# Kernel tuning notes

Measured on AMD Instinct MI355X. Metric: run time of the kernel, lower is better.

The kernel has to match this reference:

```python
import jax, jax.numpy as jnp
import numpy as np

NEG_SLOPE = 0.01  # torch F.leaky_relu default
NUM_USER, NUM_ITEM, DIM = 50000, 30000, 64
N_NODES = NUM_USER + NUM_ITEM
N_INTER = 800000
N_LAYERS = 2


def _leaky(x):
    return jax.nn.leaky_relu(x, NEG_SLOPE)


def _gcn_tower(features, preference, id_embedding, W, b, row, col):
    # x = cat(preference, features); F.normalize (L2 per row)
    x = jnp.concatenate([preference, features], axis=0)  # [N, 64]
    x = x / jnp.maximum(jnp.linalg.norm(x, axis=1, keepdims=True), 1e-12)
    deg = jax.ops.segment_sum(jnp.ones(row.shape, x.dtype), row, num_segments=N_NODES)  # bincount(row)
    for i in range(N_LAYERS):
        # Abstract_GCN: scatter-mean of gathered neighbor feats, then linear
        agg = jax.ops.segment_sum(x[col], row, num_segments=N_NODES) / deg[:, None]
        h = _leaky(agg @ W[i, 0].T + b[i, 0])
        # has_id=True, concate=False
        x_hat = _leaky(x @ W[i, 1].T + b[i, 1]) + id_embedding
        x = _leaky(h @ W[i, 2].T + b[i, 2] + x_hat)
    return x


def setup_inputs() -> dict:
    key = jax.random.key(0)
    ks = jax.random.split(key, 14)
    # bipartite user->item edges with full node coverage (every node appears
    # as a row after symmetrization, matching real interaction data where
    # bincount(row) has no zeros)
    r1 = jnp.arange(NUM_USER, dtype=jnp.int64 if jax.config.jax_enable_x64 else jnp.int32)
    c1 = jax.random.randint(ks[0], (NUM_USER,), NUM_USER, N_NODES)
    r2 = jax.random.randint(ks[1], (NUM_ITEM,), 0, NUM_USER)
    c2 = NUM_USER + jnp.arange(NUM_ITEM, dtype=r1.dtype)
    rest = N_INTER - NUM_USER - NUM_ITEM
    r3 = jax.random.randint(ks[2], (rest,), 0, NUM_USER)
    c3 = jax.random.randint(ks[3], (rest,), NUM_USER, N_NODES)
    row0 = jnp.concatenate([r1, r2, r3])
    col0 = jnp.concatenate([c1, c2, c3])
    # symmetrize: cat(edge_index, edge_index[[1,0]])
    edge_index = jnp.stack([jnp.concatenate([row0, col0]),
                            jnp.concatenate([col0, row0])])  # [2, 1.6M]
    s = 0.1  # xavier-ish scale for 64x64
    return {
        "v_feat": jax.random.normal(ks[4], (NUM_ITEM, DIM), jnp.float32),
        "t_feat": jax.random.normal(ks[5], (NUM_ITEM, DIM), jnp.float32),
        "id_embedding": jax.random.normal(ks[6], (N_NODES, DIM), jnp.float32) * s,
        "v_pref": jax.random.normal(ks[7], (NUM_USER, DIM), jnp.float32) * s,
        "t_pref": jax.random.normal(ks[8], (NUM_USER, DIM), jnp.float32) * s,
        "v_W": jax.random.normal(ks[9], (N_LAYERS, 3, DIM, DIM), jnp.float32) * s,
        "v_b": jnp.zeros((N_LAYERS, 3, DIM), jnp.float32),
        "t_W": jax.random.normal(ks[10], (N_LAYERS, 3, DIM, DIM), jnp.float32) * s,
        "t_b": jnp.zeros((N_LAYERS, 3, DIM), jnp.float32),
        "edge_index": edge_index,
    }


def reference(v_feat, t_feat, id_embedding, v_pref, t_pref, v_W, v_b, t_W, t_b, edge_index):
    row, col = edge_index[0], edge_index[1]
    rep_v = _gcn_tower(v_feat, v_pref, id_embedding, v_W, v_b, row, col)
    rep_t = _gcn_tower(t_feat, t_pref, id_embedding, t_W, t_b, row, col)
    return (rep_v + rep_t) / 2.0  # MMGCN.get_rep representation
```

## Files before the change

kernel.cpp:

```cpp
#include <hip/hip_runtime.h>
#include <hip/hip_bf16.h>

#define NUM_USER 50000
#define N_NODES  80000
#define DIM      64
#define NEG_SLOPE 0.01f

#define NB 313
#define BSHIFT 8
#define RMASK 255
#define CSHIFT 17
#define CMASK 0x1FFFF
#define CAP 10240

typedef __attribute__((ext_vector_type(8))) short short8;
typedef __attribute__((ext_vector_type(4))) float f32x4;

typedef unsigned short XT;

__device__ __forceinline__ float leaky(float v) {
    return v > 0.0f ? v : v * NEG_SLOPE;
}

__device__ __forceinline__ int load_idx(const void* ei, int is64, long long pos) {
    if (is64) return (int)((const long long*)ei)[pos];
    return ((const int*)ei)[pos];
}
__device__ __forceinline__ float load_f(const void* p, int isbf16, size_t i) {
    if (isbf16) return __bfloat162float(((const __hip_bfloat16*)p)[i]);
    return ((const float*)p)[i];
}

__device__ __forceinline__ unsigned short f2bf(float f) {
    unsigned u = __float_as_uint(f);
    u += 0x7fffu + ((u >> 16) & 1u);
    return (unsigned short)(u >> 16);
}

__device__ __forceinline__ void acc8(float* a, uint4 r) {
    a[0] += __uint_as_float(r.x << 16);
    a[1] += __uint_as_float(r.x & 0xffff0000u);
    a[2] += __uint_as_float(r.y << 16);
    a[3] += __uint_as_float(r.y & 0xffff0000u);
    a[4] += __uint_as_float(r.z << 16);
    a[5] += __uint_as_float(r.z & 0xffff0000u);
    a[6] += __uint_as_float(r.w << 16);
    a[7] += __uint_as_float(r.w & 0xffff0000u);
}

__global__ void detect_kernel(const unsigned int* __restrict__ feat_words,
                              const int* __restrict__ ei_words,
                              int* __restrict__ flags,
                              int* __restrict__ bucketCur) {
    int lane = threadIdx.x & 63;
    for (int i = lane; i < 320; i += 64) bucketCur[i] = 0;
    int orv = 0;
    for (int i = lane * 2 + 1; i < 1024; i += 128) orv |= ei_words[i];
    int hits = 0;
    for (int i = lane; i < 256; i += 64) {
        unsigned e = (feat_words[i] >> 7) & 0xFF;
        hits += (e == 126 || e == 127) ? 1 : 0;
    }
    #pragma unroll
    for (int d = 32; d > 0; d >>= 1) {
        orv  |= __shfl_xor(orv, d, 64);
        hits += __shfl_xor(hits, d, 64);
    }
    if (lane == 0 && blockIdx.x == 0) {
        flags[0] = (orv == 0) ? 1 : 0;
        flags[1] = (hits > 64) ? 1 : 0;
    }
}

__global__ __launch_bounds__(256) void megafuse_kernel(
        const void* __restrict__ ei, int E, int binBlocks, int initBlocks,
        const int* __restrict__ flags,
        int* __restrict__ bucketCur, unsigned int* __restrict__ recs,
        const void* __restrict__ vp, const void* __restrict__ tp,
        const void* __restrict__ vf, const void* __restrict__ tf,
        XT* __restrict__ xc,
        const void* __restrict__ vW, const void* __restrict__ tW,
        const void* __restrict__ vb, const void* __restrict__ tb,
        unsigned short* __restrict__ Wbf, float* __restrict__ bfp) {
    if ((int)blockIdx.x < binBlocks) {
        __shared__ int bloc[320];
        __shared__ int bres[320];
        int tid = threadIdx.x;
        for (int i = tid; i < 320; i += 256) bloc[i] = 0;
        __syncthreads();
        int is64 = flags[0];
        long long base = (long long)blockIdx.x * 2048;
        int bb[8], cc[8], lp[8], rl[8];
        #pragma unroll
        for (int it = 0; it < 8; ++it) {
            bb[it] = -1;
            long long e = base + it * 256 + tid;
            if (e < E) {
                int r = load_idx(ei, is64, e);
                int c = load_idx(ei, is64, (long long)E + e);
                if ((unsigned)r < N_NODES && (unsigned)c < N_NODES) {
                    int b = r >> BSHIFT;
                    bb[it] = b;
                    cc[it] = c;
                    rl[it] = r & RMASK;
                    lp[it] = atomicAdd(&bloc[b], 1);
                }
            }
        }
        __syncthreads();
        for (int i = tid; i < NB; i += 256) {
            int v = bloc[i];
            bres[i] = v ? atomicAdd(&bucketCur[i], v) : 0;
        }
        __syncthreads();
        #pragma unroll
        for (int it = 0; it < 8; ++it) {
            if (bb[it] >= 0) {
                int pos = bres[bb[it]] + lp[it];
                if (pos < CAP)
                    recs[(size_t)bb[it] * CAP + pos] =
                        ((unsigned)rl[it] << CSHIFT) | (unsigned)cc[it];
            }
        }
    } else if ((int)blockIdx.x < binBlocks + initBlocks) {
        int n = (blockIdx.x - binBlocks) * 4 + (threadIdx.x >> 6);
        if (n >= N_NODES) return;
        int lane = threadIdx.x & 63;
        int isb = flags[1];
        float a, b;
        if (n < NUM_USER) {
            a = load_f(vp, isb, (size_t)n * DIM + lane);
            b = load_f(tp, isb, (size_t)n * DIM + lane);
        } else {
            a = load_f(vf, isb, (size_t)(n - NUM_USER) * DIM + lane);
            b = load_f(tf, isb, (size_t)(n - NUM_USER) * DIM + lane);
        }
        float sa = a * a, sb = b * b;
        #pragma unroll
        for (int d = 32; d > 0; d >>= 1) {
            sa += __shfl_xor(sa, d, 64);
            sb += __shfl_xor(sb, d, 64);
        }
        float ra = 1.0f / fmaxf(sqrtf(sa), 1e-12f);
        float rb = 1.0f / fmaxf(sqrtf(sb), 1e-12f);
        xc[(size_t)n * 128 + lane]      = f2bf(a * ra);
        xc[(size_t)n * 128 + 64 + lane] = f2bf(b * rb);
    } else {
        int isb = flags[1];
        int j = (blockIdx.x - binBlocks - initBlocks) * 256 + threadIdx.x;
        if (j < 2 * 24576) {
            int tw = j / 24576, r = j % 24576;
            Wbf[j] = f2bf(load_f(tw ? tW : vW, isb, r));
        } else if (j < 2 * 24576 + 2 * 384) {
            int i2 = j - 2 * 24576;
            int tw = i2 / 384, r = i2 % 384;
            bfp[i2] = load_f(tw ? tb : vb, isb, r);
        }
    }
}

__global__ __launch_bounds__(512) void bin2csr_kernel(
        const unsigned int* __restrict__ recs,
        const int* __restrict__ bucketCur,
        int* __restrict__ cnt, int* __restrict__ cur,
        int* __restrict__ csr) {
    __shared__ int rcnt[256];
    __shared__ int sc[256];
    __shared__ int lcur[256];
    int b = blockIdx.x;
    int t = threadIdx.x;
    int base = b * CAP;
    int count = bucketCur[b];
    if (count > CAP) count = CAP;

    if (t < 256) { rcnt[t] = 0; lcur[t] = 0; }
    __syncthreads();
    for (int i = t; i < count; i += 512) {
        unsigned rec = recs[(size_t)base + i];
        atomicAdd(&rcnt[rec >> CSHIFT], 1);
    }
    __syncthreads();
    int v = (t < 256) ? rcnt[t] : 0;
    if (t < 256) sc[t] = v;
    __syncthreads();
    for (int d = 1; d < 256; d <<= 1) {
        int x = 0;
        if (t < 256) { x = sc[t]; if (t >= d) x += sc[t - d]; }
        __syncthreads();
        if (t < 256) sc[t] = x;
        __syncthreads();
    }
    if (t < 256) {
        int row = (b << BSHIFT) + t;
        if (row < N_NODES) {
            cnt[row] = v;
            cur[row] = base + sc[t];
        }
    }
    __syncthreads();
    for (int i = t; i < count; i += 512) {
        unsigned rec = recs[(size_t)base + i];
        int rloc = rec >> CSHIFT;
        int c = rec & CMASK;
        int pos = base + (sc[rloc] - rcnt[rloc]) + atomicAdd(&lcur[rloc], 1);
        csr[pos] = c;
    }
}

__global__ __launch_bounds__(512) void gather_kernel(
        const XT* __restrict__ xc, XT* __restrict__ agg,
        const int* __restrict__ cnt, const int* __restrict__ cur,
        const int* __restrict__ csr) {
    int n = blockIdx.x * 8 + (threadIdx.x >> 6);
    if (n >= N_NODES) return;
    int lane = threadIdx.x & 63;
    int g8 = lane >> 3;
    int s  = lane & 7;
    int gg = g8 >> 1;
    int h  = g8 & 1;

    int d = cnt[n];
    int base = cur[n] - d;
    const int* nb = csr + base;
    const XT* xh = xc + h * 64;

    float acc[8];
    #pragma unroll
    for (int f = 0; f < 8; ++f) acc[f] = 0.f;

    int jj = gg;
    for (; jj + 4 < d; jj += 8) {
        int c0 = nb[jj];
        int c1 = nb[jj + 4];
        uint4 r0 = ((const uint4*)(xh + (size_t)c0 * 128))[s];
        uint4 r1 = ((const uint4*)(xh + (size_t)c1 * 128))[s];
        acc8(acc, r0);
        acc8(acc, r1);
    }
    if (jj < d) {
        int c0 = nb[jj];
        uint4 r0 = ((const uint4*)(xh + (size_t)c0 * 128))[s];
        acc8(acc, r0);
    }

    #pragma unroll
    for (int dd = 16; dd < 64; dd <<= 1) {
        #pragma unroll
        for (int f = 0; f < 8; ++f) acc[f] += __shfl_xor(acc[f], dd, 64);
    }

    float invd = (d > 0) ? 1.0f / (float)d : 0.0f;
    if (g8 < 2) {
        uint4 w;
        w.x = (unsigned)f2bf(acc[0] * invd) | ((unsigned)f2bf(acc[1] * invd) << 16);
        w.y = (unsigned)f2bf(acc[2] * invd) | ((unsigned)f2bf(acc[3] * invd) << 16);
        w.z = (unsigned)f2bf(acc[4] * invd) | ((unsigned)f2bf(acc[5] * invd) << 16);
        w.w = (unsigned)f2bf(acc[6] * invd) | ((unsigned)f2bf(acc[7] * invd) << 16);
        ((uint4*)(agg + (size_t)n * 128 + h * 64))[s] = w;
    }
}

__global__ __launch_bounds__(256) void dense_mfma_kernel(
        XT* __restrict__ xc, const XT* __restrict__ agg,
        void* __restrict__ out, int last,
        const void* __restrict__ id_emb,
        const unsigned short* __restrict__ Wbf, const float* __restrict__ bfp,
        int layer, const int* __restrict__ flags) {
    __shared__ unsigned short hts[4][16 * 72];
    int wave = threadIdx.x >> 6, lane = threadIdx.x & 63;
    int quad = lane >> 4, l16 = lane & 15;
    int isb = flags[1];
    int n0 = (blockIdx.x * 4 + wave) * 16;
    unsigned short* ht = hts[wave];

    float xres[2][16];
    float idv[16];

    #pragma unroll
    for (int tw = 0; tw < 2; ++tw) {
        int toff = tw * 64;
        const unsigned short* Wm = Wbf + (size_t)((tw * 2 + layer) * 3) * 4096;
        const float* bb = bfp + (tw * 2 + layer) * 192;
        size_t arow = (size_t)(n0 + l16) * 128 + toff + quad * 8;

        short8 a0, a1;
        f32x4 accP[4];

        a0 = *(const short8*)(xc + arow);
        a1 = *(const short8*)(xc + arow + 32);
        #pragma unroll
        for (int t = 0; t < 4; ++t) {
            f32x4 c = {0.f, 0.f, 0.f, 0.f};
            short8 b0 = *(const short8*)(Wm + 4096 + (16 * t + l16) * 64 + quad * 8);
            short8 b1 = *(const short8*)(Wm + 4096 + (16 * t + l16) * 64 + 32 + quad * 8);
            c = __builtin_amdgcn_mfma_f32_16x16x32_bf16(a0, b0, c, 0, 0, 0);
            c = __builtin_amdgcn_mfma_f32_16x16x32_bf16(a1, b1, c, 0, 0, 0);
            float bias = bb[64 + 16 * t + l16];
            #pragma unroll
            for (int r = 0; r < 4; ++r) accP[t][r] = leaky(c[r] + bias);
        }

        a0 = *(const short8*)(agg + arow);
        a1 = *(const short8*)(agg + arow + 32);
        #pragma unroll
        for (int t = 0; t < 4; ++t) {
            f32x4 c = {0.f, 0.f, 0.f, 0.f};
            short8 b0 = *(const short8*)(Wm + (16 * t + l16) * 64 + quad * 8);
            short8 b1 = *(const short8*)(Wm + (16 * t + l16) * 64 + 32 + quad * 8);
            c = __builtin_amdgcn_mfma_f32_16x16x32_bf16(a0, b0, c, 0, 0, 0);
            c = __builtin_amdgcn_mfma_f32_16x16x32_bf16(a1, b1, c, 0, 0, 0);
            float bias = bb[16 * t + l16];
            #pragma unroll
            for (int r = 0; r < 4; ++r)
                ht[(quad * 4 + r) * 72 + 16 * t + l16] = f2bf(leaky(c[r] + bias));
        }

        a0 = *(const short8*)(ht + l16 * 72 + quad * 8);
        a1 = *(const short8*)(ht + l16 * 72 + 32 + quad * 8);
        #pragma unroll
        for (int t = 0; t < 4; ++t) {
            f32x4 c = {0.f, 0.f, 0.f, 0.f};
            short8 b0 = *(const short8*)(Wm + 2 * 4096 + (16 * t + l16) * 64 + quad * 8);
            short8 b1 = *(const short8*)(Wm + 2 * 4096 + (16 * t + l16) * 64 + 32 + quad * 8);
            c = __builtin_amdgcn_mfma_f32_16x16x32_bf16(a0, b0, c, 0, 0, 0);
            c = __builtin_amdgcn_mfma_f32_16x16x32_bf16(a1, b1, c, 0, 0, 0);
            float bias = bb[128 + 16 * t + l16];
            #pragma unroll
            for (int r = 0; r < 4; ++r) {
                int node2 = n0 + quad * 4 + r;
                int j = 16 * t + l16;
                if (tw == 0)
                    idv[t * 4 + r] = load_f(id_emb, isb, (size_t)node2 * 64 + j);
                xres[tw][t * 4 + r] = leaky(c[r] + bias + accP[t][r] + idv[t * 4 + r]);
            }
        }
    }

    if (!last) {
        #pragma unroll
        for (int tw = 0; tw < 2; ++tw) {
            #pragma unroll
            for (int t = 0; t < 4; ++t) {
                #pragma unroll
                for (int r = 0; r < 4; ++r) {
                    int node2 = n0 + quad * 4 + r;
                    int j = 16 * t + l16;
                    xc[(size_t)node2 * 128 + tw * 64 + j] = f2bf(xres[tw][t * 4 + r]);
                }
            }
        }
    } else {
        #pragma unroll
        for (int t = 0; t < 4; ++t) {
            #pragma unroll
            for (int r = 0; r < 4; ++r) {
                int node2 = n0 + quad * 4 + r;
                int j = 16 * t + l16;
                float avg = (xres[0][t * 4 + r] + xres[1][t * 4 + r]) * 0.5f;
                if (isb) ((unsigned short*)out)[(size_t)node2 * 64 + j] = f2bf(avg);
                else     ((float*)out)[(size_t)node2 * 64 + j] = avg;
            }
        }
    }
}

extern "C" void kernel_launch(void* const* d_in, const int* in_sizes, int n_in,
                              void* d_out, int out_size, void* d_ws, size_t ws_size,
                              hipStream_t stream) {
    const void* v_feat = d_in[0];
    const void* t_feat = d_in[1];
    const void* id_emb = d_in[2];
    const void* v_pref = d_in[3];
    const void* t_pref = d_in[4];
    const void* v_W    = d_in[5];
    const void* v_b    = d_in[6];
    const void* t_W    = d_in[7];
    const void* t_b    = d_in[8];
    const void* ei     = d_in[9];

    const int E = in_sizes[9] / 2;
    char* ws = (char*)d_ws;

    size_t o = 0;
    int*            flags     = (int*)(ws + o);            o += 16;
    int*            cnt       = (int*)(ws + o);            o += 320000;
    int*            cur       = (int*)(ws + o);            o += 320000;
    int*            bucketCur = (int*)(ws + o);            o += 320 * 4;
    unsigned short* Wbf       = (unsigned short*)(ws + o); o += 2 * 24576 * 2;
    float*          bfp       = (float*)(ws + o);          o += 2 * 384 * 4;
    XT* xc  = (XT*)(ws + o); o += (size_t)N_NODES * 128 * sizeof(XT);
    XT* agg = (XT*)(ws + o); o += (size_t)N_NODES * 128 * sizeof(XT);
    unsigned int* recs = (unsigned int*)(ws + o); o += (size_t)NB * CAP * 4;
    int* csr = (int*)(ws + o);

    detect_kernel<<<dim3(1), dim3(64), 0, stream>>>(
        (const unsigned int*)v_feat, (const int*)ei, flags, bucketCur);

    const int binBlocks  = (E + 2047) / 2048;
    const int initBlocks = (N_NODES + 3) / 4;
    const int packBlocks = (2 * 24576 + 2 * 384 + 255) / 256;
    megafuse_kernel<<<dim3(binBlocks + initBlocks + packBlocks), dim3(256), 0, stream>>>(
        ei, E, binBlocks, initBlocks, flags, bucketCur, recs,
        v_pref, t_pref, v_feat, t_feat, xc,
        v_W, t_W, v_b, t_b, Wbf, bfp);

    bin2csr_kernel<<<dim3(NB), dim3(512), 0, stream>>>(recs, bucketCur, cnt, cur, csr);

    const int gatherBlocks = (N_NODES + 7) / 8;
    const int denseBlocks  = N_NODES / (16 * 4);

    gather_kernel<<<dim3(gatherBlocks), dim3(512), 0, stream>>>(xc, agg, cnt, cur, csr);
    dense_mfma_kernel<<<dim3(denseBlocks), dim3(256), 0, stream>>>(
        xc, agg, d_out, 0, id_emb, Wbf, bfp, 0, flags);
    gather_kernel<<<dim3(gatherBlocks), dim3(512), 0, stream>>>(xc, agg, cnt, cur, csr);
    dense_mfma_kernel<<<dim3(denseBlocks), dim3(256), 0, stream>>>(
        xc, agg, d_out, 1, id_emb, Wbf, bfp, 1, flags);
}
```

Before: 365.4 us.

## Fuse neighbor gather into dense MFMA layer kernel with ping-pong buffers

Merges the gather (scatter-mean) kernel into the dense MFMA kernel. Each wave aggregates its 16 nodes into shared memory, then runs the linear layers directly from LDS. Features are double-buffered (xcA/xcB) because other blocks may still be reading the old features while the layer writes new ones. This removes the agg round trip through global memory and two launches. The cost is less gather parallelism per node, since each wave now handles 16 nodes in sequence. Also widens bin2csr to 1024 threads, and adds a redundant bias store line.

After: 458.4 us. +25.5%, slower.

```diff
diff --git a/kernel.cpp b/kernel.cpp
--- a/kernel.cpp
+++ b/kernel.cpp
@@ -154,12 +154,12 @@
         } else if (j < 2 * 24576 + 2 * 384) {
             int i2 = j - 2 * 24576;
             int tw = i2 / 384, r = i2 % 384;
-            bfp[i2] = load_f(tw ? tb : vb, isb, r);
-        }
-    }
-}
-
-__global__ __launch_bounds__(512) void bin2csr_kernel(
+            bfp[i2] = f2bf(0.0f), bfp[i2] = load_f(tw ? tb : vb, isb, r);
+        }
+    }
+}
+
+__global__ __launch_bounds__(1024) void bin2csr_kernel(
         const unsigned int* __restrict__ recs,
         const int* __restrict__ bucketCur,
         int* __restrict__ cnt, int* __restrict__ cur,
@@ -175,7 +175,7 @@
 
     if (t < 256) { rcnt[t] = 0; lcur[t] = 0; }
     __syncthreads();
-    for (int i = t; i < count; i += 512) {
+    for (int i = t; i < count; i += 1024) {
         unsigned rec = recs[(size_t)base + i];
         atomicAdd(&rcnt[rec >> CSHIFT], 1);
     }
@@ -198,7 +198,7 @@
         }
     }
     __syncthreads();
-    for (int i = t; i < count; i += 512) {
+    for (int i = t; i < count; i += 1024) {
         unsigned rec = recs[(size_t)base + i];
         int rloc = rec >> CSHIFT;
         int c = rec & CMASK;
@@ -207,74 +207,73 @@
     }
 }
 
-__global__ __launch_bounds__(512) void gather_kernel(
-        const XT* __restrict__ xc, XT* __restrict__ agg,
-        const int* __restrict__ cnt, const int* __restrict__ cur,
-        const int* __restrict__ csr) {
-    int n = blockIdx.x * 8 + (threadIdx.x >> 6);
-    if (n >= N_NODES) return;
-    int lane = threadIdx.x & 63;
-    int g8 = lane >> 3;
-    int s  = lane & 7;
-    int gg = g8 >> 1;
-    int h  = g8 & 1;
-
-    int d = cnt[n];
-    int base = cur[n] - d;
-    const int* nb = csr + base;
-    const XT* xh = xc + h * 64;
-
-    float acc[8];
-    #pragma unroll
-    for (int f = 0; f < 8; ++f) acc[f] = 0.f;
-
-    int jj = gg;
-    for (; jj + 4 < d; jj += 8) {
-        int c0 = nb[jj];
-        int c1 = nb[jj + 4];
-        uint4 r0 = ((const uint4*)(xh + (size_t)c0 * 128))[s];
-        uint4 r1 = ((const uint4*)(xh + (size_t)c1 * 128))[s];
-        acc8(acc, r0);
-        acc8(acc, r1);
-    }
-    if (jj < d) {
-        int c0 = nb[jj];
-        uint4 r0 = ((const uint4*)(xh + (size_t)c0 * 128))[s];
-        acc8(acc, r0);
-    }
-
-    #pragma unroll
-    for (int dd = 16; dd < 64; dd <<= 1) {
-        #pragma unroll
-        for (int f = 0; f < 8; ++f) acc[f] += __shfl_xor(acc[f], dd, 64);
-    }
-
-    float invd = (d > 0) ? 1.0f / (float)d : 0.0f;
-    if (g8 < 2) {
-        uint4 w;
-        w.x = (unsigned)f2bf(acc[0] * invd) | ((unsigned)f2bf(acc[1] * invd) << 16);
-        w.y = (unsigned)f2bf(acc[2] * invd) | ((unsigned)f2bf(acc[3] * invd) << 16);
-        w.z = (unsigned)f2bf(acc[4] * invd) | ((unsigned)f2bf(acc[5] * invd) << 16);
-        w.w = (unsigned)f2bf(acc[6] * invd) | ((unsigned)f2bf(acc[7] * invd) << 16);
-        ((uint4*)(agg + (size_t)n * 128 + h * 64))[s] = w;
-    }
-}
-
-__global__ __launch_bounds__(256) void dense_mfma_kernel(
-        XT* __restrict__ xc, const XT* __restrict__ agg,
+__global__ __launch_bounds__(256) void layer_fused_kernel(
+        const XT* __restrict__ xin, XT* __restrict__ xout,
         void* __restrict__ out, int last,
         const void* __restrict__ id_emb,
         const unsigned short* __restrict__ Wbf, const float* __restrict__ bfp,
+        const int* __restrict__ cnt, const int* __restrict__ cur,
+        const int* __restrict__ csr,
         int layer, const int* __restrict__ flags) {
+    __shared__ unsigned short aggs[4][16 * 136];
     __shared__ unsigned short hts[4][16 * 72];
     int wave = threadIdx.x >> 6, lane = threadIdx.x & 63;
     int quad = lane >> 4, l16 = lane & 15;
     int isb = flags[1];
     int n0 = (blockIdx.x * 4 + wave) * 16;
-    unsigned short* ht = hts[wave];
-
-    float xres[2][16];
-    float idv[16];
+    unsigned short* agg = aggs[wave];
+    unsigned short* ht  = hts[wave];
+
+    {
+        int g8 = lane >> 3;
+        int s  = lane & 7;
+        int gg = g8 >> 1;
+        int h  = g8 & 1;
+        const XT* xh = xin + h * 64;
+
+        for (int k = 0; k < 16; ++k) {
+            int node = n0 + k;
+            int d = cnt[node];
+            int base = cur[node] - d;
+            const int* nb = csr + base;
+
+            float acc[8];
+            #pragma unroll
+            for (int f = 0; f < 8; ++f) acc[f] = 0.f;
+
+            int jj = gg;
+            for (; jj + 4 < d; jj += 8) {
+                int c0 = nb[jj];
+                int c1 = nb[jj + 4];
+                uint4 r0 = ((const uint4*)(xh + (size_t)c0 * 128))[s];
+                uint4 r1 = ((const uint4*)(xh + (size_t)c1 * 128))[s];
+                acc8(acc, r0);
+                acc8(acc, r1);
+            }
+            if (jj < d) {
+                uint4 r0 = ((const uint4*)(xh + (size_t)nb[jj] * 128))[s];
+                acc8(acc, r0);
+            }
+
+            #pragma unroll
+            for (int dd = 16; dd < 64; dd <<= 1) {
+                #pragma unroll
+                for (int f = 0; f < 8; ++f) acc[f] += __shfl_xor(acc[f], dd, 64);
+            }
+
+            float invd = (d > 0) ? 1.0f / (float)d : 0.0f;
+            if (g8 < 2) {
+                uint4 w;
+                w.x = (unsigned)f2bf(acc[0] * invd) | ((unsigned)f2bf(acc[1] * invd) << 16);
+                w.y = (unsigned)f2bf(acc[2] * invd) | ((unsigned)f2bf(acc[3] * invd) << 16);
+                w.z = (unsigned)f2bf(acc[4] * invd) | ((unsigned)f2bf(acc[5] * invd) << 16);
+                w.w = (unsigned)f2bf(acc[6] * invd) | ((unsigned)f2bf(acc[7] * invd) << 16);
+                *(uint4*)(agg + k * 136 + h * 64 + s * 8) = w;
+            }
+        }
+    }
+
+    float res0[16];
 
     #pragma unroll
     for (int tw = 0; tw < 2; ++tw) {
@@ -286,8 +285,8 @@
         short8 a0, a1;
         f32x4 accP[4];
 
-        a0 = *(const short8*)(xc + arow);
-        a1 = *(const short8*)(xc + arow + 32);
+        a0 = *(const short8*)(xin + arow);
+        a1 = *(const short8*)(xin + arow + 32);
         #pragma unroll
         for (int t = 0; t < 4; ++t) {
             f32x4 c = {0.f, 0.f, 0.f, 0.f};
@@ -300,8 +299,8 @@
             for (int r = 0; r < 4; ++r) accP[t][r] = leaky(c[r] + bias);
         }
 
-        a0 = *(const short8*)(agg + arow);
-        a1 = *(const short8*)(agg + arow + 32);
+        a0 = *(const short8*)(agg + l16 * 136 + toff + quad * 8);
+        a1 = *(const short8*)(agg + l16 * 136 + toff + 32 + quad * 8);
         #pragma unroll
         for (int t = 0; t < 4; ++t) {
             f32x4 c = {0.f, 0.f, 0.f, 0.f};
@@ -329,36 +328,17 @@
             for (int r = 0; r < 4; ++r) {
                 int node2 = n0 + quad * 4 + r;
                 int j = 16 * t + l16;
-                if (tw == 0)
-                    idv[t * 4 + r] = load_f(id_emb, isb, (size_t)node2 * 64 + j);
-                xres[tw][t * 4 + r] = leaky(c[r] + bias + accP[t][r] + idv[t * 4 + r]);
-            }
-        }
-    }
-
-    if (!last) {
-        #pragma unroll
-        for (int tw = 0; tw < 2; ++tw) {
-            #pragma unroll
-            for (int t = 0; t < 4; ++t) {
-                #pragma unroll
-                for (int r = 0; r < 4; ++r) {
-                    int node2 = n0 + quad * 4 + r;
-                    int j = 16 * t + l16;
-                    xc[(size_t)node2 * 128 + tw * 64 + j] = f2bf(xres[tw][t * 4 + r]);
+                float idv = load_f(id_emb, isb, (size_t)node2 * 64 + j);
+                float v = leaky(c[r] + bias + accP[t][r] + idv);
+                if (!last) {
+                    xout[(size_t)node2 * 128 + toff + j] = f2bf(v);
+                } else if (tw == 0) {
+                    res0[t * 4 + r] = v;
+                } else {
+                    float avg = (res0[t * 4 + r] + v) * 0.5f;
+                    if (isb) ((unsigned short*)out)[(size_t)node2 * 64 + j] = f2bf(avg);
+                    else     ((float*)out)[(size_t)node2 * 64 + j] = avg;
                 }
-            }
-        }
-    } else {
-        #pragma unroll
-        for (int t = 0; t < 4; ++t) {
-            #pragma unroll
-            for (int r = 0; r < 4; ++r) {
-                int node2 = n0 + quad * 4 + r;
-                int j = 16 * t + l16;
-                float avg = (xres[0][t * 4 + r] + xres[1][t * 4 + r]) * 0.5f;
-                if (isb) ((unsigned short*)out)[(size_t)node2 * 64 + j] = f2bf(avg);
-                else     ((float*)out)[(size_t)node2 * 64 + j] = avg;
             }
         }
     }
@@ -388,8 +368,8 @@
     int*            bucketCur = (int*)(ws + o);            o += 320 * 4;
     unsigned short* Wbf       = (unsigned short*)(ws + o); o += 2 * 24576 * 2;
     float*          bfp       = (float*)(ws + o);          o += 2 * 384 * 4;
-    XT* xc  = (XT*)(ws + o); o += (size_t)N_NODES * 128 * sizeof(XT);
-    XT* agg = (XT*)(ws + o); o += (size_t)N_NODES * 128 * sizeof(XT);
+    XT* xcA = (XT*)(ws + o); o += (size_t)N_NODES * 128 * sizeof(XT);
+    XT* xcB = (XT*)(ws + o); o += (size_t)N_NODES * 128 * sizeof(XT);
     unsigned int* recs = (unsigned int*)(ws + o); o += (size_t)NB * CAP * 4;
     int* csr = (int*)(ws + o);
 
@@ -401,18 +381,15 @@
     const int packBlocks = (2 * 24576 + 2 * 384 + 255) / 256;
     megafuse_kernel<<<dim3(binBlocks + initBlocks + packBlocks), dim3(256), 0, stream>>>(
         ei, E, binBlocks, initBlocks, flags, bucketCur, recs,
-        v_pref, t_pref, v_feat, t_feat, xc,
+        v_pref, t_pref, v_feat, t_feat, xcA,
         v_W, t_W, v_b, t_b, Wbf, bfp);
 
-    bin2csr_kernel<<<dim3(NB), dim3(512), 0, stream>>>(recs, bucketCur, cnt, cur, csr);
-
-    const int gatherBlocks = (N_NODES + 7) / 8;
-    const int denseBlocks  = N_NODES / (16 * 4);
-
-    gather_kernel<<<dim3(gatherBlocks), dim3(512), 0, stream>>>(xc, agg, cnt, cur, csr);
-    dense_mfma_kernel<<<dim3(denseBlocks), dim3(256), 0, stream>>>(
-        xc, agg, d_out, 0, id_emb, Wbf, bfp, 0, flags);
-    gather_kernel<<<dim3(gatherBlocks), dim3(512), 0, stream>>>(xc, agg, cnt, cur, csr);
-    dense_mfma_kernel<<<dim3(denseBlocks), dim3(256), 0, stream>>>(
-        xc, agg, d_out, 1, id_emb, Wbf, bfp, 1, flags);
-}
+    bin2csr_kernel<<<dim3(NB), dim3(1024), 0, stream>>>(recs, bucketCur, cnt, cur, csr);
+
+    const int layerBlocks = N_NODES / (16 * 4);
+
+    layer_fused_kernel<<<dim3(layerBlocks), dim3(256), 0, stream>>>(
+        xcA, xcB, d_out, 0, id_emb, Wbf, bfp, cnt, cur, csr, 0, flags);
+    layer_fused_kernel<<<dim3(layerBlocks), dim3(256), 0, stream>>>(
+        xcB, xcA, d_out, 1, id_emb, Wbf, bfp, cnt, cur, csr, 1, flags);
+}
```

## Regroup prep kernels and pre-convert id embedding to bf16

Applied to the files above, without the earlier changes.

Splits the edge binning into its own kernel and merges the bucket-to-CSR pass with feature normalization and weight packing in one 512-thread launch. The independent init and pack work can then overlap with CSR construction. When workspace allows, the id embedding is also converted to bf16 once so the dense kernels read half the bytes. This adds an 80000x64 conversion pass and rounds id_embedding to bf16, which slightly lowers precision.

After: 381.3 us. 1.04x slower.

```diff
diff --git a/kernel.cpp b/kernel.cpp
--- a/kernel.cpp
+++ b/kernel.cpp
@@ -35,6 +35,9 @@
     unsigned u = __float_as_uint(f);
     u += 0x7fffu + ((u >> 16) & 1u);
     return (unsigned short)(u >> 16);
+}
+__device__ __forceinline__ float bf2f(unsigned short v) {
+    return __uint_as_float(((unsigned)v) << 16);
 }
 
 __device__ __forceinline__ void acc8(float* a, uint4 r) {
@@ -72,58 +75,108 @@
     }
 }
 
-__global__ __launch_bounds__(256) void megafuse_kernel(
-        const void* __restrict__ ei, int E, int binBlocks, int initBlocks,
+__global__ __launch_bounds__(256) void binplace_kernel(
+        const void* __restrict__ ei, int E,
         const int* __restrict__ flags,
-        int* __restrict__ bucketCur, unsigned int* __restrict__ recs,
+        int* __restrict__ bucketCur, unsigned int* __restrict__ recs) {
+    __shared__ int bloc[320];
+    __shared__ int bres[320];
+    int tid = threadIdx.x;
+    for (int i = tid; i < 320; i += 256) bloc[i] = 0;
+    __syncthreads();
+    int is64 = flags[0];
+    long long base = (long long)blockIdx.x * 2048;
+    int bb[8], cc[8], lp[8], rl[8];
+    #pragma unroll
+    for (int it = 0; it < 8; ++it) {
+        bb[it] = -1;
+        long long e = base + it * 256 + tid;
+        if (e < E) {
+            int r = load_idx(ei, is64, e);
+            int c = load_idx(ei, is64, (long long)E + e);
+            if ((unsigned)r < N_NODES && (unsigned)c < N_NODES) {
+                int b = r >> BSHIFT;
+                bb[it] = b;
+                cc[it] = c;
+                rl[it] = r & RMASK;
+                lp[it] = atomicAdd(&bloc[b], 1);
+            }
+        }
+    }
+    __syncthreads();
+    for (int i = tid; i < NB; i += 256) {
+        int v = bloc[i];
+        bres[i] = v ? atomicAdd(&bucketCur[i], v) : 0;
+    }
+    __syncthreads();
+    #pragma unroll
+    for (int it = 0; it < 8; ++it) {
+        if (bb[it] >= 0) {
+            int pos = bres[bb[it]] + lp[it];
+            if (pos < CAP)
+                recs[(size_t)bb[it] * CAP + pos] =
+                    ((unsigned)rl[it] << CSHIFT) | (unsigned)cc[it];
+        }
+    }
+}
+
+__global__ __launch_bounds__(512) void prep2_kernel(
+        const unsigned int* __restrict__ recs, const int* __restrict__ bucketCur,
+        int* __restrict__ cnt, int* __restrict__ cur, int* __restrict__ csr,
+        int initBlocks, const int* __restrict__ flags,
         const void* __restrict__ vp, const void* __restrict__ tp,
         const void* __restrict__ vf, const void* __restrict__ tf,
         XT* __restrict__ xc,
         const void* __restrict__ vW, const void* __restrict__ tW,
         const void* __restrict__ vb, const void* __restrict__ tb,
-        unsigned short* __restrict__ Wbf, float* __restrict__ bfp) {
-    if ((int)blockIdx.x < binBlocks) {
-        __shared__ int bloc[320];
-        __shared__ int bres[320];
-        int tid = threadIdx.x;
-        for (int i = tid; i < 320; i += 256) bloc[i] = 0;
+        unsigned short* __restrict__ Wbf, float* __restrict__ bfp,
+        const void* __restrict__ id_emb, unsigned short* __restrict__ idbf,
+        int useIdbf) {
+    int bx = blockIdx.x;
+    if (bx < NB) {
+        __shared__ int rcnt[256];
+        __shared__ int sc[256];
+        __shared__ int lcur[256];
+        int b = bx;
+        int t = threadIdx.x;
+        int base = b * CAP;
+        int count = bucketCur[b];
+        if (count > CAP) count = CAP;
+
+        if (t < 256) { rcnt[t] = 0; lcur[t] = 0; }
         __syncthreads();
-        int is64 = flags[0];
-        long long base = (long long)blockIdx.x * 2048;
-        int bb[8], cc[8], lp[8], rl[8];
-        #pragma unroll
-        for (int it = 0; it < 8; ++it) {
-            bb[it] = -1;
-            long long e = base + it * 256 + tid;
-            if (e < E) {
-                int r = load_idx(ei, is64, e);
-                int c = load_idx(ei, is64, (long long)E + e);
-                if ((unsigned)r < N_NODES && (unsigned)c < N_NODES) {
-                    int b = r >> BSHIFT;
-                    bb[it] = b;
-                    cc[it] = c;
-                    rl[it] = r & RMASK;
-                    lp[it] = atomicAdd(&bloc[b], 1);
-                }
+        for (int i = t; i < count; i += 512) {
+            unsigned rec = recs[(size_t)base + i];
+            atomicAdd(&rcnt[rec >> CSHIFT], 1);
+        }
+        __syncthreads();
+        int v = (t < 256) ? rcnt[t] : 0;
+        if (t < 256) sc[t] = v;
+        __syncthreads();
+        for (int d = 1; d < 256; d <<= 1) {
+            int x = 0;
+            if (t < 256) { x = sc[t]; if (t >= d) x += sc[t - d]; }
+            __syncthreads();
+            if (t < 256) sc[t] = x;
+            __syncthreads();
+        }
+        if (t < 256) {
+            int row = (b << BSHIFT) + t;
+            if (row < N_NODES) {
+                cnt[row] = v;
+                cur[row] = base + sc[t];
             }
         }
         __syncthreads();
-        for (int i = tid; i < NB; i += 256) {
-            int v = bloc[i];
-            bres[i] = v ? atomicAdd(&bucketCur[i], v) : 0;
-        }
-        __syncthreads();
-        #pragma unroll
-        for (int it = 0; it < 8; ++it) {
-            if (bb[it] >= 0) {
-                int pos = bres[bb[it]] + lp[it];
-                if (pos < CAP)
-                    recs[(size_t)bb[it] * CAP + pos] =
-                        ((unsigned)rl[it] << CSHIFT) | (unsigned)cc[it];
-            }
-        }
-    } else if ((int)blockIdx.x < binBlocks + initBlocks) {
-        int n = (blockIdx.x - binBlocks) * 4 + (threadIdx.x >> 6);
+        for (int i = t; i < count; i += 512) {
+            unsigned rec = recs[(size_t)base + i];
+            int rloc = rec >> CSHIFT;
+            int c = rec & CMASK;
+            int pos = base + (sc[rloc] - rcnt[rloc]) + atomicAdd(&lcur[rloc], 1);
+            csr[pos] = c;
+        }
+    } else if (bx < NB + initBlocks) {
+        int n = (bx - NB) * 8 + (threadIdx.x >> 6);
         if (n >= N_NODES) return;
         int lane = threadIdx.x & 63;
         int isb = flags[1];
@@ -147,7 +200,7 @@
         xc[(size_t)n * 128 + 64 + lane] = f2bf(b * rb);
     } else {
         int isb = flags[1];
-        int j = (blockIdx.x - binBlocks - initBlocks) * 256 + threadIdx.x;
+        int j = (bx - NB - initBlocks) * 512 + threadIdx.x;
         if (j < 2 * 24576) {
             int tw = j / 24576, r = j % 24576;
             Wbf[j] = f2bf(load_f(tw ? tW : vW, isb, r));
@@ -155,55 +208,11 @@
             int i2 = j - 2 * 24576;
             int tw = i2 / 384, r = i2 % 384;
             bfp[i2] = load_f(tw ? tb : vb, isb, r);
-        }
-    }
-}
-
-__global__ __launch_bounds__(512) void bin2csr_kernel(
-        const unsigned int* __restrict__ recs,
-        const int* __restrict__ bucketCur,
-        int* __restrict__ cnt, int* __restrict__ cur,
-        int* __restrict__ csr) {
-    __shared__ int rcnt[256];
-    __shared__ int sc[256];
-    __shared__ int lcur[256];
-    int b = blockIdx.x;
-    int t = threadIdx.x;
-    int base = b * CAP;
-    int count = bucketCur[b];
-    if (count > CAP) count = CAP;
-
-    if (t < 256) { rcnt[t] = 0; lcur[t] = 0; }
-    __syncthreads();
-    for (int i = t; i < count; i += 512) {
-        unsigned rec = recs[(size_t)base + i];
-        atomicAdd(&rcnt[rec >> CSHIFT], 1);
-    }
-    __syncthreads();
-    int v = (t < 256) ? rcnt[t] : 0;
-    if (t < 256) sc[t] = v;
-    __syncthreads();
-    for (int d = 1; d < 256; d <<= 1) {
-        int x = 0;
-        if (t < 256) { x = sc[t]; if (t >= d) x += sc[t - d]; }
-        __syncthreads();
-        if (t < 256) sc[t] = x;
-        __syncthreads();
-    }
-    if (t < 256) {
-        int row = (b << BSHIFT) + t;
-        if (row < N_NODES) {
-            cnt[row] = v;
-            cur[row] = base + sc[t];
-        }
-    }
-    __syncthreads();
-    for (int i = t; i < count; i += 512) {
-        unsigned rec = recs[(size_t)base + i];
-        int rloc = rec >> CSHIFT;
-        int c = rec & CMASK;
-        int pos = base + (sc[rloc] - rcnt[rloc]) + atomicAdd(&lcur[rloc], 1);
-        csr[pos] = c;
+        } else if (useIdbf) {
+            int k = j - (2 * 24576 + 2 * 384);
+            if (k < N_NODES * DIM)
+                idbf[k] = f2bf(load_f(id_emb, isb, (size_t)k));
+        }
     }
 }
 
@@ -263,7 +272,7 @@
 __global__ __launch_bounds__(256) void dense_mfma_kernel(
         XT* __restrict__ xc, const XT* __restrict__ agg,
         void* __restrict__ out, int last,
-        const void* __restrict__ id_emb,
+        const void* __restrict__ id_emb, const unsigned short* __restrict__ idbf,
         const unsigned short* __restrict__ Wbf, const float* __restrict__ bfp,
         int layer, const int* __restrict__ flags) {
     __shared__ unsigned short hts[4][16 * 72];
@@ -330,7 +339,8 @@
                 int node2 = n0 + quad * 4 + r;
                 int j = 16 * t + l16;
                 if (tw == 0)
-                    idv[t * 4 + r] = load_f(id_emb, isb, (size_t)node2 * 64 + j);
+                    idv[t * 4 + r] = idbf ? bf2f(idbf[(size_t)node2 * 64 + j])
+                                          : load_f(id_emb, isb, (size_t)node2 * 64 + j);
                 xres[tw][t * 4 + r] = leaky(c[r] + bias + accP[t][r] + idv[t * 4 + r]);
             }
         }
@@ -391,28 +401,38 @@
     XT* xc  = (XT*)(ws + o); o += (size_t)N_NODES * 128 * sizeof(XT);
     XT* agg = (XT*)(ws + o); o += (size_t)N_NODES * 128 * sizeof(XT);
     unsigned int* recs = (unsigned int*)(ws + o); o += (size_t)NB * CAP * 4;
-    int* csr = (int*)(ws + o);
+    int* csr = (int*)(ws + o);                     o += (size_t)NB * CAP * 4;
+    unsigned short* idbf = nullptr;
+    int useIdbf = 0;
+    if (o + (size_t)N_NODES * DIM * 2 <= ws_size) {
+        idbf = (unsigned short*)(ws + o);
+        useIdbf = 1;
+    }
 
     detect_kernel<<<dim3(1), dim3(64), 0, stream>>>(
         (const unsigned int*)v_feat, (const int*)ei, flags, bucketCur);
 
-    const int binBlocks  = (E + 2047) / 2048;
-    const int initBlocks = (N_NODES + 3) / 4;
-    const int packBlocks = (2 * 24576 + 2 * 384 + 255) / 256;
-    megafuse_kernel<<<dim3(binBlocks + initBlocks + packBlocks), dim3(256), 0, stream>>>(
-        ei, E, binBlocks, initBlocks, flags, bucketCur, recs,
+    const int binBlocks = (E + 2047) / 2048;
+    binplace_kernel<<<dim3(binBlocks), dim3(256), 0, stream>>>(
+        ei, E, flags, bucketCur, recs);
+
+    const int initBlocks = (N_NODES + 7) / 8;
+    const int packElems  = 2 * 24576 + 2 * 384 + (useIdbf ? N_NODES * DIM : 0);
+    const int packBlocks = (packElems + 511) / 512;
+    prep2_kernel<<<dim3(NB + initBlocks + packBlocks), dim3(512), 0, stream>>>(
+        recs, bucketCur, cnt, cur, csr,
+        initBlocks, flags,
         v_pref, t_pref, v_feat, t_feat, xc,
-        v_W, t_W, v_b, t_b, Wbf, bfp);
-
-    bin2csr_kernel<<<dim3(NB), dim3(512), 0, stream>>>(recs, bucketCur, cnt, cur, csr);
+        v_W, t_W, v_b, t_b, Wbf, bfp,
+        id_emb, idbf, useIdbf);
 
     const int gatherBlocks = (N_NODES + 7) / 8;
     const int denseBlocks  = N_NODES / (16 * 4);
 
     gather_kernel<<<dim3(gatherBlocks), dim3(512), 0, stream>>>(xc, agg, cnt, cur, csr);
     dense_mfma_kernel<<<dim3(denseBlocks), dim3(256), 0, stream>>>(
-        xc, agg, d_out, 0, id_emb, Wbf, bfp, 0, flags);
+        xc, agg, d_out, 0, id_emb, idbf, Wbf, bfp, 0, flags);
     gather_kernel<<<dim3(gatherBlocks), dim3(512), 0, stream>>>(xc, agg, cnt, cur, csr);
     dense_mfma_kernel<<<dim3(denseBlocks), dim3(256), 0, stream>>>(
-        xc, agg, d_out, 1, id_emb, Wbf, bfp, 1, flags);
-}
+        xc, agg, d_out, 1, id_emb, idbf, Wbf, bfp, 1, flags);
+}
```

## Split dense MFMA work across towers per wave and widen bin2csr blocks

Applied to the files above, without the earlier changes.

The dense kernel now gives each wave a single tower for a 16-node tile instead of both towers serially. Blocks cover 32 nodes, doubling wave-level parallelism and shortening each wave's dependent chain. In the last layer the tower-1 results are shared through LDS so tower-0 waves can average them, which adds a block barrier and extra shared memory. Separately, bin2csr blocks grow from 512 to 1024 threads so each bucket's records are processed with more threads.

Result: no change. 365.5 us (+0.0%).

```diff
diff --git a/kernel.cpp b/kernel.cpp
--- a/kernel.cpp
+++ b/kernel.cpp
@@ -159,7 +159,7 @@
     }
 }
 
-__global__ __launch_bounds__(512) void bin2csr_kernel(
+__global__ __launch_bounds__(1024) void bin2csr_kernel(
         const unsigned int* __restrict__ recs,
         const int* __restrict__ bucketCur,
         int* __restrict__ cnt, int* __restrict__ cur,
@@ -175,7 +175,7 @@
 
     if (t < 256) { rcnt[t] = 0; lcur[t] = 0; }
     __syncthreads();
-    for (int i = t; i < count; i += 512) {
+    for (int i = t; i < count; i += 1024) {
         unsigned rec = recs[(size_t)base + i];
         atomicAdd(&rcnt[rec >> CSHIFT], 1);
     }
@@ -198,7 +198,7 @@
         }
     }
     __syncthreads();
-    for (int i = t; i < count; i += 512) {
+    for (int i = t; i < count; i += 1024) {
         unsigned rec = recs[(size_t)base + i];
         int rloc = rec >> CSHIFT;
         int c = rec & CMASK;
@@ -267,98 +267,107 @@
         const unsigned short* __restrict__ Wbf, const float* __restrict__ bfp,
         int layer, const int* __restrict__ flags) {
     __shared__ unsigned short hts[4][16 * 72];
+    __shared__ float res[2][16][65];
     int wave = threadIdx.x >> 6, lane = threadIdx.x & 63;
     int quad = lane >> 4, l16 = lane & 15;
+    int tile  = wave >> 1;
+    int tower = wave & 1;
     int isb = flags[1];
-    int n0 = (blockIdx.x * 4 + wave) * 16;
+    int n0 = (blockIdx.x * 2 + tile) * 16;
+    int toff = tower * 64;
+    const unsigned short* Wm = Wbf + (size_t)((tower * 2 + layer) * 3) * 4096;
+    const float* bb = bfp + (tower * 2 + layer) * 192;
     unsigned short* ht = hts[wave];
 
-    float xres[2][16];
+    size_t arow = (size_t)(n0 + l16) * 128 + toff + quad * 8;
+
+    short8 x0  = *(const short8*)(xc + arow);
+    short8 x1  = *(const short8*)(xc + arow + 32);
+    short8 ga0 = *(const short8*)(agg + arow);
+    short8 ga1 = *(const short8*)(agg + arow + 32);
+
+    f32x4 accP[4];
+
+    #pragma unroll
+    for (int t = 0; t < 4; ++t) {
+        f32x4 c = {0.f, 0.f, 0.f, 0.f};
+        short8 b0 = *(const short8*)(Wm + 4096 + (16 * t + l16) * 64 + quad * 8);
+        short8 b1 = *(const short8*)(Wm + 4096 + (16 * t + l16) * 64 + 32 + quad * 8);
+        c = __builtin_amdgcn_mfma_f32_16x16x32_bf16(x0, b0, c, 0, 0, 0);
+        c = __builtin_amdgcn_mfma_f32_16x16x32_bf16(x1, b1, c, 0, 0, 0);
+        float bias = bb[64 + 16 * t + l16];
+        #pragma unroll
+        for (int r = 0; r < 4; ++r) accP[t][r] = leaky(c[r] + bias);
+    }
+
+    #pragma unroll
+    for (int t = 0; t < 4; ++t) {
+        f32x4 c = {0.f, 0.f, 0.f, 0.f};
+        short8 b0 = *(const short8*)(Wm + (16 * t + l16) * 64 + quad * 8);
+        short8 b1 = *(const short8*)(Wm + (16 * t + l16) * 64 + 32 + quad * 8);
+        c = __builtin_amdgcn_mfma_f32_16x16x32_bf16(ga0, b0, c, 0, 0, 0);
+        c = __builtin_amdgcn_mfma_f32_16x16x32_bf16(ga1, b1, c, 0, 0, 0);
+        float bias = bb[16 * t + l16];
+        #pragma unroll
+        for (int r = 0; r < 4; ++r)
+            ht[(quad * 4 + r) * 72 + 16 * t + l16] = f2bf(leaky(c[r] + bias));
+    }
+
     float idv[16];
-
-    #pragma unroll
-    for (int tw = 0; tw < 2; ++tw) {
-        int toff = tw * 64;
-        const unsigned short* Wm = Wbf + (size_t)((tw * 2 + layer) * 3) * 4096;
-        const float* bb = bfp + (tw * 2 + layer) * 192;
-        size_t arow = (size_t)(n0 + l16) * 128 + toff + quad * 8;
-
-        short8 a0, a1;
-        f32x4 accP[4];
-
-        a0 = *(const short8*)(xc + arow);
-        a1 = *(const short8*)(xc + arow + 32);
+    #pragma unroll
+    for (int t = 0; t < 4; ++t)
+        #pragma unroll
+        for (int r = 0; r < 4; ++r)
+            idv[t * 4 + r] = load_f(id_emb, isb,
+                                    (size_t)(n0 + quad * 4 + r) * 64 + 16 * t + l16);
+
+    short8 a0 = *(const short8*)(ht + l16 * 72 + quad * 8);
+    short8 a1 = *(const short8*)(ht + l16 * 72 + 32 + quad * 8);
+
+    float xres[16];
+    #pragma unroll
+    for (int t = 0; t < 4; ++t) {
+        f32x4 c = {0.f, 0.f, 0.f, 0.f};
+        short8 b0 = *(const short8*)(Wm + 2 * 4096 + (16 * t + l16) * 64 + quad * 8);
+        short8 b1 = *(const short8*)(Wm + 2 * 4096 + (16 * t + l16) * 64 + 32 + quad * 8);
+        c = __builtin_amdgcn_mfma_f32_16x16x32_bf16(a0, b0, c, 0, 0, 0);
+        c = __builtin_amdgcn_mfma_f32_16x16x32_bf16(a1, b1, c, 0, 0, 0);
+        float bias = bb[128 + 16 * t + l16];
+        #pragma unroll
+        for (int r = 0; r < 4; ++r)
+            xres[t * 4 + r] = leaky(c[r] + bias + accP[t][r] + idv[t * 4 + r]);
+    }
+
+    if (!last) {
         #pragma unroll
         for (int t = 0; t < 4; ++t) {
-            f32x4 c = {0.f, 0.f, 0.f, 0.f};
-            short8 b0 = *(const short8*)(Wm + 4096 + (16 * t + l16) * 64 + quad * 8);
-            short8 b1 = *(const short8*)(Wm + 4096 + (16 * t + l16) * 64 + 32 + quad * 8);
-            c = __builtin_amdgcn_mfma_f32_16x16x32_bf16(a0, b0, c, 0, 0, 0);
-            c = __builtin_amdgcn_mfma_f32_16x16x32_bf16(a1, b1, c, 0, 0, 0);
-            float bias = bb[64 + 16 * t + l16];
-            #pragma unroll
-            for (int r = 0; r < 4; ++r) accP[t][r] = leaky(c[r] + bias);
-        }
-
-        a0 = *(const short8*)(agg + arow);
-        a1 = *(const short8*)(agg + arow + 32);
-        #pragma unroll
-        for (int t = 0; t < 4; ++t) {
-            f32x4 c = {0.f, 0.f, 0.f, 0.f};
-            short8 b0 = *(const short8*)(Wm + (16 * t + l16) * 64 + quad * 8);
-            short8 b1 = *(const short8*)(Wm + (16 * t + l16) * 64 + 32 + quad * 8);
-            c = __builtin_amdgcn_mfma_f32_16x16x32_bf16(a0, b0, c, 0, 0, 0);
-            c = __builtin_amdgcn_mfma_f32_16x16x32_bf16(a1, b1, c, 0, 0, 0);
-            float bias = bb[16 * t + l16];
-            #pragma unroll
-            for (int r = 0; r < 4; ++r)
-                ht[(quad * 4 + r) * 72 + 16 * t + l16] = f2bf(leaky(c[r] + bias));
-        }
-
-        a0 = *(const short8*)(ht + l16 * 72 + quad * 8);
-        a1 = *(const short8*)(ht + l16 * 72 + 32 + quad * 8);
-        #pragma unroll
-        for (int t = 0; t < 4; ++t) {
-            f32x4 c = {0.f, 0.f, 0.f, 0.f};
-            short8 b0 = *(const short8*)(Wm + 2 * 4096 + (16 * t + l16) * 64 + quad * 8);
-            short8 b1 = *(const short8*)(Wm + 2 * 4096 + (16 * t + l16) * 64 + 32 + quad * 8);
-            c = __builtin_amdgcn_mfma_f32_16x16x32_bf16(a0, b0, c, 0, 0, 0);
-            c = __builtin_amdgcn_mfma_f32_16x16x32_bf16(a1, b1, c, 0, 0, 0);
-            float bias = bb[128 + 16 * t + l16];
             #pragma unroll
             for (int r = 0; r < 4; ++r) {
                 int node2 = n0 + quad * 4 + r;
                 int j = 16 * t + l16;
-                if (tw == 0)
-                    idv[t * 4 + r] = load_f(id_emb, isb, (size_t)node2 * 64 + j);
-                xres[tw][t * 4 + r] = leaky(c[r] + bias + accP[t][r] + idv[t * 4 + r]);
+                xc[(size_t)node2 * 128 + toff + j] = f2bf(xres[t * 4 + r]);
             }
         }
-    }
-
-    if (!last) {
-        #pragma unroll
-        for (int tw = 0; tw < 2; ++tw) {
+    } else {
+        if (tower == 1) {
+            #pragma unroll
+            for (int t = 0; t < 4; ++t)
+                #pragma unroll
+                for (int r = 0; r < 4; ++r)
+                    res[tile][quad * 4 + r][16 * t + l16] = xres[t * 4 + r];
+        }
+        __syncthreads();
+        if (tower == 0) {
             #pragma unroll
             for (int t = 0; t < 4; ++t) {
                 #pragma unroll
                 for (int r = 0; r < 4; ++r) {
                     int node2 = n0 + quad * 4 + r;
                     int j = 16 * t + l16;
-                    xc[(size_t)node2 * 128 + tw * 64 + j] = f2bf(xres[tw][t * 4 + r]);
+                    float avg = (xres[t * 4 + r] + res[tile][quad * 4 + r][j]) * 0.5f;
+                    if (isb) ((unsigned short*)out)[(size_t)node2 * 64 + j] = f2bf(avg);
+                    else     ((float*)out)[(size_t)node2 * 64 + j] = avg;
                 }
-            }
-        }
-    } else {
-        #pragma unroll
-        for (int t = 0; t < 4; ++t) {
-            #pragma unroll
-            for (int r = 0; r < 4; ++r) {
-                int node2 = n0 + quad * 4 + r;
-                int j = 16 * t + l16;
-                float avg = (xres[0][t * 4 + r] + xres[1][t * 4 + r]) * 0.5f;
-                if (isb) ((unsigned short*)out)[(size_t)node2 * 64 + j] = f2bf(avg);
-                else     ((float*)out)[(size_t)node2 * 64 + j] = avg;
             }
         }
     }
@@ -404,10 +413,10 @@
         v_pref, t_pref, v_feat, t_feat, xc,
         v_W, t_W, v_b, t_b, Wbf, bfp);
 
-    bin2csr_kernel<<<dim3(NB), dim3(512), 0, stream>>>(recs, bucketCur, cnt, cur, csr);
+    bin2csr_kernel<<<dim3(NB), dim3(1024), 0, stream>>>(recs, bucketCur, cnt, cur, csr);
 
     const int gatherBlocks = (N_NODES + 7) / 8;
-    const int denseBlocks  = N_NODES / (16 * 4);
+    const int denseBlocks  = N_NODES / 32;
 
     gather_kernel<<<dim3(gatherBlocks), dim3(512), 0, stream>>>(xc, agg, cnt, cur, csr);
     dense_mfma_kernel<<<dim3(denseBlocks), dim3(256), 0, stream>>>(
```
